# Performance work log

Hardware: AMD Instinct MI355X
Metric: run time of the kernel (lower is better)

## Reference

```python
import jax, jax.numpy as jnp
import numpy as np

EPS = 1e-8  # torch F.cosine_similarity eps


def setup_inputs() -> dict:
    key = jax.random.key(0)
    ks = jax.random.split(key, 12)
    B, S, D, C, V = 2, 1024, 512, 1000, 50000
    sc = lambda fan_in: 1.0 / np.sqrt(fan_in)
    return {
        "spectrum_real": jax.random.normal(ks[0], (B, S, D), jnp.float32),
        "spectrum_imag": jax.random.normal(ks[1], (B, S, D), jnp.float32),
        "concept_spectra_real": jax.random.normal(ks[2], (C, D), jnp.float32),
        "concept_spectra_imag": jax.random.normal(ks[3], (C, D), jnp.float32),
        "W1": jax.random.normal(ks[4], (2 * D, D), jnp.float32) * sc(2 * D),
        "b1": jnp.zeros((D,), jnp.float32),
        "W2": jax.random.normal(ks[5], (D, 512), jnp.float32) * sc(D),
        "b2": jnp.zeros((512,), jnp.float32),
        "W3": jax.random.normal(ks[6], (512, 768), jnp.float32) * sc(512),
        "b3": jnp.zeros((768,), jnp.float32),
        "W4": jax.random.normal(ks[7], (768, V), jnp.float32) * sc(768),
        "b4": jnp.zeros((V,), jnp.float32),
        "top_k": 5,
    }


def reference(spectrum_real, spectrum_imag, concept_spectra_real, concept_spectra_imag,
              W1, b1, W2, b2, W3, b3, W4, b4, top_k):
    # --- find_spectral_matches: batched cosine similarity over magnitudes + top-k ---
    mag = jnp.sqrt(spectrum_real ** 2 + spectrum_imag ** 2)            # [B,S,D]
    cmag = jnp.sqrt(concept_spectra_real ** 2 + concept_spectra_imag ** 2)  # [C,D]
    # cosine sim = (x . y) / (max(||x||, eps) * max(||y||, eps))
    dots = jnp.einsum('bsd,cd->bsc', mag, cmag)                        # [B,S,C]
    xn = jnp.maximum(jnp.linalg.norm(mag, axis=-1), EPS)               # [B,S]
    yn = jnp.maximum(jnp.linalg.norm(cmag, axis=-1), EPS)              # [C]
    sims = dots / (xn[..., None] * yn[None, None, :])                  # [B,S,C]
    top_sims, top_idx = jax.lax.top_k(sims, top_k)                     # [B,S,k]

    # --- decode_spectral_concepts: cat(real, imag) -> MLP -> vocab logits ---
    gelu = lambda x: jax.nn.gelu(x, approximate=False)                 # torch nn.GELU default
    x = jnp.concatenate([spectrum_real, spectrum_imag], axis=-1)       # [B,S,2D]
    h = gelu(x @ W1 + b1)
    h = gelu(h @ W2 + b2)
    h = gelu(h @ W3 + b3)
    logits = h @ W4 + b4                                               # [B,S,V]
    return top_sims, top_idx, logits
```

## Files before the change

### kernel.cpp

```cpp
#include <hip/hip_runtime.h>
#include <hip/hip_bf16.h>
#include <hip/hip_fp8.h>

#define CEPS 1e-8f

typedef __attribute__((ext_vector_type(8))) __bf16 bf16x8;
typedef __attribute__((ext_vector_type(4))) float f32x4;

__device__ __forceinline__ void gload_lds16(const void* g, void* l) {
  __builtin_amdgcn_global_load_lds((const __attribute__((address_space(1))) unsigned int*)g,
                                   (__attribute__((address_space(3))) unsigned int*)l, 16, 0, 0);
}

__device__ __forceinline__ float gelu_f(float v) {
  return 0.5f * v * (1.0f + erff(v * 0.70710678118654752f));
}

__device__ __forceinline__ unsigned char f32_to_e4m3(float v) {
  __hip_fp8_e4m3 t(v);
  return (unsigned char)t.__x;
}


__device__ __forceinline__ void dev_mag(double* red, const float* __restrict__ re,
                                        const float* __restrict__ im, float* __restrict__ mag,
                                        __hip_bfloat16* __restrict__ xcat, float* __restrict__ xn,
                                        int row) {
  const float* r = re + (size_t)row * 512;
  const float* q = im + (size_t)row * 512;
  double ss = 0.0;
  for (int d = threadIdx.x; d < 512; d += 256) {
    float a = r[d], b = q[d];
    float s = __fadd_rn(__fmul_rn(a, a), __fmul_rn(b, b));
    float m = __fsqrt_rn(s);
    mag[(size_t)row * 512 + d] = m;
    xcat[(size_t)row * 1024 + d] = __float2bfloat16(a);
    xcat[(size_t)row * 1024 + 512 + d] = __float2bfloat16(b);
    ss += (double)m * (double)m;
  }
  for (int off = 32; off; off >>= 1) ss += __shfl_xor(ss, off);
  int lane = threadIdx.x & 63, wave = threadIdx.x >> 6;
  if (lane == 0) red[wave] = ss;
  __syncthreads();
  if (threadIdx.x == 0) {
    double tot = red[0] + red[1] + red[2] + red[3];
    float n = (float)sqrt(tot);
    xn[row] = fmaxf(n, CEPS);
  }
}

__device__ __forceinline__ void dev_cmag(double* red, const float* __restrict__ cre,
                                         const float* __restrict__ cim, float* __restrict__ cmagT,
                                         float* __restrict__ yn, int c) {
  const float* r = cre + (size_t)c * 512;
  const float* q = cim + (size_t)c * 512;
  double ss = 0.0;
  for (int d = threadIdx.x; d < 512; d += 256) {
    float a = r[d], b = q[d];
    float s = __fadd_rn(__fmul_rn(a, a), __fmul_rn(b, b));
    float m = __fsqrt_rn(s);
    cmagT[(size_t)d * 1000 + c] = m;
    ss += (double)m * (double)m;
  }
  for (int off = 32; off; off >>= 1) ss += __shfl_xor(ss, off);
  int lane = threadIdx.x & 63, wave = threadIdx.x >> 6;
  if (lane == 0) red[wave] = ss;
  __syncthreads();
  if (threadIdx.x == 0) {
    double tot = red[0] + red[1] + red[2] + red[3];
    float n = (float)sqrt(tot);
    yn[c] = fmaxf(n, CEPS);
  }
}

template <int OUTT>
__device__ __forceinline__ void dev_tr(float (*t32)[65], const float* __restrict__ W,
                                       void* __restrict__ Wt, int K, int N, int bx, int by) {
  int n0 = bx * 64, k0 = by * 64;
  int tid = threadIdx.x;
  {
    int nc = tid & 15, kr4 = tid >> 4;
#pragma unroll
    for (int p = 0; p < 4; ++p) {
      int kr = p * 16 + kr4;
      int n = n0 + nc * 4;
      float4 v = make_float4(0.f, 0.f, 0.f, 0.f);
      if (n < N) v = *(const float4*)(W + (size_t)(k0 + kr) * N + n);
      t32[kr][nc * 4 + 0] = v.x; t32[kr][nc * 4 + 1] = v.y;
      t32[kr][nc * 4 + 2] = v.z; t32[kr][nc * 4 + 3] = v.w;
    }
  }
  __syncthreads();
  {
    int kc = tid & 15, nr4 = tid >> 4;
#pragma unroll
    for (int p = 0; p < 4; ++p) {
      int nr = p * 16 + nr4;
      if (OUTT == 0) {
        ushort4 o;
        __hip_bfloat16 h0 = __float2bfloat16(t32[kc * 4 + 0][nr]);
        __hip_bfloat16 h1 = __float2bfloat16(t32[kc * 4 + 1][nr]);
        __hip_bfloat16 h2 = __float2bfloat16(t32[kc * 4 + 2][nr]);
        __hip_bfloat16 h3 = __float2bfloat16(t32[kc * 4 + 3][nr]);
        o.x = *(unsigned short*)&h0; o.y = *(unsigned short*)&h1;
        o.z = *(unsigned short*)&h2; o.w = *(unsigned short*)&h3;
        *(ushort4*)((unsigned short*)Wt + (size_t)(n0 + nr) * K + k0 + kc * 4) = o;
      } else {
        unsigned int o = (unsigned int)f32_to_e4m3(t32[kc * 4 + 0][nr]) |
                         ((unsigned int)f32_to_e4m3(t32[kc * 4 + 1][nr]) << 8) |
                         ((unsigned int)f32_to_e4m3(t32[kc * 4 + 2][nr]) << 16) |
                         ((unsigned int)f32_to_e4m3(t32[kc * 4 + 3][nr]) << 24);
        *(unsigned int*)((unsigned char*)Wt + (size_t)(n0 + nr) * K + k0 + kc * 4) = o;
      }
    }
  }
}

template <int OUTT>
__device__ __forceinline__ void dev_mlp(short* Al, short* Bl, const __hip_bfloat16* __restrict__ A,
                                        const __hip_bfloat16* __restrict__ Bt, void* __restrict__ C,
                                        int M, int N, int K, int ldc, const float* __restrict__ bias,
                                        int bx, int by) {
  const int tid = threadIdx.x, lane = tid & 63, wave = tid >> 6;
  const int m0 = by * 128, n0 = bx * 128;
  const int wr = wave >> 1, wc = wave & 1;
  f32x4 acc[4][4];
  f32x4 zero4 = {0.f, 0.f, 0.f, 0.f};
#pragma unroll
  for (int i = 0; i < 4; ++i)
#pragma unroll
    for (int j = 0; j < 4; ++j) acc[i][j] = zero4;

  const short* Ag = (const short*)A;
  const short* Bg = (const short*)Bt;
  for (int k0 = 0; k0 < K; k0 += 32) {
#pragma unroll
    for (int s = 0; s < 2; ++s) {
      int seg = wave + s * 4;
      int elem = seg * 512 + lane * 8;
      int row = elem >> 5, kk = elem & 31;
      gload_lds16(Ag + (size_t)(m0 + row) * K + k0 + kk, Al + elem);
      gload_lds16(Bg + (size_t)(n0 + row) * K + k0 + kk, Bl + elem);
    }
    __syncthreads();
    bf16x8 af[4], bfr[4];
    const int fr = lane & 15, fk = (lane >> 4) << 3;
#pragma unroll
    for (int i = 0; i < 4; ++i)
      af[i] = *(const bf16x8*)(Al + (wr * 64 + i * 16 + fr) * 32 + fk);
#pragma unroll
    for (int j = 0; j < 4; ++j)
      bfr[j] = *(const bf16x8*)(Bl + (wc * 64 + j * 16 + fr) * 32 + fk);
#pragma unroll
    for (int i = 0; i < 4; ++i)
#pragma unroll
      for (int j = 0; j < 4; ++j)
        acc[i][j] = __builtin_amdgcn_mfma_f32_16x16x32_bf16(af[i], bfr[j], acc[i][j], 0, 0, 0);
    __syncthreads();
  }
  const int fr = lane & 15, fq = lane >> 4;
#pragma unroll
  for (int j = 0; j < 4; ++j) {
    int col = n0 + wc * 64 + j * 16 + fr;
    if (col >= N) continue;
    float bv = bias[col];
#pragma unroll
    for (int i = 0; i < 4; ++i) {
      int rbase = m0 + wr * 64 + i * 16 + fq * 4;
#pragma unroll
      for (int r = 0; r < 4; ++r) {
        float v = gelu_f(acc[i][j][r] + bv);
        if (OUTT == 0)
          ((__hip_bfloat16*)C)[(size_t)(rbase + r) * ldc + col] = __float2bfloat16(v);
        else
          ((unsigned char*)C)[(size_t)(rbase + r) * ldc + col] = f32_to_e4m3(v);
      }
    }
  }
}

__device__ __forceinline__ void dev_dots(double (*As)[64], double (*Bs)[64],
                                         const float* __restrict__ A, const float* __restrict__ Bm,
                                         float* __restrict__ Cm, int M, int N, int K, int ldc,
                                         const float* __restrict__ xn, const float* __restrict__ yn,
                                         int nb, int mb) {
  const int tid = threadIdx.x;
  const int m0 = mb * 64, n0 = nb * 64;
  const int tx = tid & 15, ty4 = tid >> 4;
  const int ar = tid >> 2, ak = (tid & 3) << 2;
  const int bk = tid >> 4, bn = (tid & 15) << 2;
  double acc[4][4] = {};
  for (int k0 = 0; k0 < K; k0 += 16) {
    float4 a4 = *(const float4*)(A + (size_t)(m0 + ar) * K + k0 + ak);
    As[ak + 0][ar] = (double)a4.x; As[ak + 1][ar] = (double)a4.y;
    As[ak + 2][ar] = (double)a4.z; As[ak + 3][ar] = (double)a4.w;
    float4 b4 = make_float4(0.f, 0.f, 0.f, 0.f);
    if (n0 + bn < N) b4 = *(const float4*)(Bm + (size_t)(k0 + bk) * N + n0 + bn);
    Bs[bk][bn + 0] = (double)b4.x; Bs[bk][bn + 1] = (double)b4.y;
    Bs[bk][bn + 2] = (double)b4.z; Bs[bk][bn + 3] = (double)b4.w;
    __syncthreads();
#pragma unroll
    for (int kk = 0; kk < 16; ++kk) {
      double av[4], bv[4];
#pragma unroll
      for (int i = 0; i < 4; ++i) av[i] = As[kk][ty4 + i * 16];
#pragma unroll
      for (int j = 0; j < 4; ++j) bv[j] = Bs[kk][tx + j * 16];
#pragma unroll
      for (int i = 0; i < 4; ++i)
#pragma unroll
        for (int j = 0; j < 4; ++j)
          acc[i][j] = fma(av[i], bv[j], acc[i][j]);
    }
    __syncthreads();
  }
#pragma unroll
  for (int i = 0; i < 4; ++i) {
    int row = m0 + ty4 + i * 16;
#pragma unroll
    for (int j = 0; j < 4; ++j) {
      int col = n0 + tx + j * 16;
      if (col >= N) continue;
      double d = acc[i][j] / ((double)xn[row] * (double)yn[col]);
      Cm[(size_t)row * ldc + col] = (float)d;
    }
  }
}

__device__ __forceinline__ void dev_gemm(unsigned char (*As)[16384], unsigned char (*Bs)[8192],
                                         const unsigned char* __restrict__ A8,
                                         const unsigned char* __restrict__ B8,
                                         float* __restrict__ C, const float* __restrict__ bias,
                                         int xcd, int j) {
  const int KNT = 12;
  const int Kd = 768, Nd = 50000, ldc = 50000;
  const int tid = threadIdx.x, lane = tid & 63, wave = tid >> 6;
  const int wm = wave >> 1, wn = wave & 1;

  const int mt = j & 7;
  const int ntile = xcd + 8 * (j >> 3);
  const int m0 = mt * 256, n0 = ntile * 128;

  f32x4 acc[8][4];
  f32x4 z4 = {0.f, 0.f, 0.f, 0.f};
#pragma unroll
  for (int q = 0; q < 8; ++q)
#pragma unroll
    for (int p = 0; p < 4; ++p) acc[q][p] = z4;

  auto stageA = [&](int kt, int buf) {
    if (kt >= KNT) return;
    const int k0 = kt * 64;
#pragma unroll
    for (int r = 0; r < 4; ++r) {
      int idx = r * 256 + tid;
      int row = idx >> 2, c = idx & 3;
      int src = ((c * 2) ^ (row & 6)) * 8;
      gload_lds16(A8 + (size_t)(m0 + row) * Kd + k0 + src, &As[buf][row * 64 + c * 16]);
    }
  };
  auto stageB = [&](int kt, int buf) {
    if (kt >= KNT) return;
    const int k0 = kt * 64;
#pragma unroll
    for (int r = 0; r < 2; ++r) {
      int idx = r * 256 + tid;
      int row = idx >> 2, c = idx & 3;
      int src = ((c * 2) ^ (row & 6)) * 8;
      gload_lds16(B8 + (size_t)(n0 + row) * Kd + k0 + src, &Bs[buf][row * 64 + c * 16]);
    }
  };

  stageA(0, 0); stageB(0, 0);
  stageA(1, 1); stageB(1, 1);

  for (int g = 0; g < KNT; ++g) {
    const int buf = g & 1;
    if (g < KNT - 1) asm volatile("s_waitcnt vmcnt(6)" ::: "memory");
    else             asm volatile("s_waitcnt vmcnt(0)" ::: "memory");
    __builtin_amdgcn_sched_barrier(0);
    __builtin_amdgcn_s_barrier();
    __builtin_amdgcn_sched_barrier(0);

    long bfr[4][2];
#pragma unroll
    for (int p = 0; p < 4; ++p) {
      int row = wn * 64 + p * 16 + (lane & 15);
#pragma unroll
      for (int kh = 0; kh < 2; ++kh) {
        int slot = (kh * 4 + (lane >> 4)) ^ (row & 6);
        bfr[p][kh] = *(const long*)(&Bs[buf][row * 64 + slot * 8]);
      }
    }
    __builtin_amdgcn_s_setprio(1);
#pragma unroll
    for (int q = 0; q < 8; ++q) {
      int rowA = wm * 128 + q * 16 + (lane & 15);
      long af[2];
#pragma unroll
      for (int kh = 0; kh < 2; ++kh) {
        int slot = (kh * 4 + (lane >> 4)) ^ (rowA & 6);
        af[kh] = *(const long*)(&As[buf][rowA * 64 + slot * 8]);
      }
#pragma unroll
      for (int kh = 0; kh < 2; ++kh)
#pragma unroll
        for (int p = 0; p < 4; ++p)
          acc[q][p] = __builtin_amdgcn_mfma_f32_16x16x32_fp8_fp8(bfr[p][kh], af[kh], acc[q][p], 0, 0, 0);
    }
    __builtin_amdgcn_s_setprio(0);

    __builtin_amdgcn_sched_barrier(0);
    __builtin_amdgcn_s_barrier();
    __builtin_amdgcn_sched_barrier(0);
    stageA(g + 2, buf);
    stageB(g + 2, buf);
  }

  const int colq = (lane >> 4) * 4;
  float4 bias4[4];
#pragma unroll
  for (int p = 0; p < 4; ++p) {
    int colbase = n0 + wn * 64 + p * 16 + colq;
    bias4[p] = (colbase < Nd) ? *(const float4*)(bias + colbase) : make_float4(0.f, 0.f, 0.f, 0.f);
  }
#pragma unroll
  for (int q = 0; q < 8; ++q) {
    int row = m0 + wm * 128 + q * 16 + (lane & 15);
#pragma unroll
    for (int p = 0; p < 4; ++p) {
      int colbase = n0 + wn * 64 + p * 16 + colq;
      if (colbase < Nd) {
        f32x4 v = acc[q][p];
        float4 o = make_float4(v[0] + bias4[p].x, v[1] + bias4[p].y,
                               v[2] + bias4[p].z, v[3] + bias4[p].w);
        *(float4*)(&C[(size_t)row * ldc + colbase]) = o;
      }
    }
  }
}


__global__ __launch_bounds__(256) void k_pre(const float* W1, __hip_bfloat16* w1t,
                                             const float* W2, __hip_bfloat16* w2t,
                                             const float* W3, __hip_bfloat16* w3t,
                                             const float* cre, const float* cim, float* cmagT, float* yn,
                                             const float* sre, const float* simg, float* mag,
                                             __hip_bfloat16* xcat, float* xn) {
  __shared__ float t32[64][65];
  __shared__ double red[4];
  int bid = blockIdx.x;
  if (bid < 128) {
    dev_tr<0>(t32, W1, (void*)w1t, 1024, 512, bid & 7, bid >> 3);
  } else if (bid < 192) {
    int t = bid - 128;
    dev_tr<0>(t32, W2, (void*)w2t, 512, 512, t & 7, t >> 3);
  } else if (bid < 288) {
    int t = bid - 192;
    dev_tr<0>(t32, W3, (void*)w3t, 512, 768, t % 12, t / 12);
  } else if (bid < 1288) {
    dev_cmag(red, cre, cim, cmagT, yn, bid - 288);
  } else {
    dev_mag(red, sre, simg, mag, xcat, xn, bid - 1288);
  }
}

__global__ __launch_bounds__(256) void k_l1w4(const __hip_bfloat16* xcat, const __hip_bfloat16* w1t,
                                              __hip_bfloat16* h1b, const float* b1,
                                              const float* W4, unsigned char* w4f8) {
  __shared__ short Al[128 * 32];
  __shared__ short Bl[128 * 32];
  __shared__ float t32[64][65];
  int bid = blockIdx.x;
  if (bid < 64) {
    dev_mlp<0>(Al, Bl, xcat, w1t, (void*)h1b, 2048, 512, 1024, 512, b1, bid & 3, bid >> 2);
  } else {
    int t = bid - 64;
    dev_tr<1>(t32, W4, (void*)w4f8, 768, 50000, t % 784, t / 784);
  }
}

template <int OUTT>
__global__ __launch_bounds__(256) void k_mlp(const __hip_bfloat16* A, const __hip_bfloat16* Bt,
                                             void* C, int M, int N, int K, int ldc, const float* bias) {
  __shared__ short Al[128 * 32];
  __shared__ short Bl[128 * 32];
  dev_mlp<OUTT>(Al, Bl, A, Bt, C, M, N, K, ldc, bias, blockIdx.x, blockIdx.y);
}

union KMainSmem {
  struct { unsigned char As[2][16384]; unsigned char Bs[2][8192]; } g;
  struct { double As[16][64]; double Bs[16][64]; } d;
};

__global__ __launch_bounds__(256, 2) void k_main(const unsigned char* __restrict__ A8,
                                                 const unsigned char* __restrict__ B8,
                                                 float* __restrict__ C, const float* __restrict__ bias,
                                                 const float* __restrict__ mag,
                                                 const float* __restrict__ cmagT,
                                                 float* __restrict__ simsb,
                                                 const float* __restrict__ xn,
                                                 const float* __restrict__ yn) {
  __shared__ KMainSmem sm;
  const int bid = blockIdx.x;
  const int g = bid >> 3;
  const bool isDots = ((g % 7) == 3) && (g <= 444);
  if (isDots) {
    int dgi = (g - 3) / 7;
    int id = dgi * 8 + (bid & 7);
    dev_dots(sm.d.As, sm.d.Bs, mag, cmagT, simsb, 2048, 1000, 512, 1000, xn, yn,
             id & 15, id >> 4);
  } else {
    int dots_before = (g < 3) ? 0 : min(64, (g + 4) / 7);
    int jg = g - dots_before;
    dev_gemm(sm.g.As, sm.g.Bs, A8, B8, C, bias, bid & 7, jg);
  }
}

__global__ __launch_bounds__(256) void k_topk(const float* __restrict__ sims,
                                              float* __restrict__ top_sims, float* __restrict__ top_idx) {
  int lane = threadIdx.x & 63, wave = threadIdx.x >> 6;
  int row = blockIdx.x * 4 + wave;
  const float* s = sims + (size_t)row * 1000;
  float v[16];
  int idx[16];
#pragma unroll
  for (int t = 0; t < 16; ++t) {
    int c = lane + t * 64;
    if (c < 1000) { v[t] = s[c]; idx[t] = c; }
    else { v[t] = -1e30f; idx[t] = 1 << 20; }
  }
  for (int j = 0; j < 5; ++j) {
    float bv = -1e30f; int bi = 1 << 20;
#pragma unroll
    for (int t = 0; t < 16; ++t) {
      if (v[t] > bv || (v[t] == bv && idx[t] < bi)) { bv = v[t]; bi = idx[t]; }
    }
    float rv = bv; int ri = bi;
#pragma unroll
    for (int off = 32; off; off >>= 1) {
      float ov = __shfl_xor(rv, off);
      int oi = __shfl_xor(ri, off);
      if (ov > rv || (ov == rv && oi < ri)) { rv = ov; ri = oi; }
    }
    if (lane == 0) {
      top_sims[(size_t)row * 5 + j] = rv;
      top_idx[(size_t)row * 5 + j] = (float)ri;
    }
#pragma unroll
    for (int t = 0; t < 16; ++t)
      if (idx[t] == ri) v[t] = -1e30f;
  }
}

extern "C" void kernel_launch(void* const* d_in, const int* in_sizes, int n_in,
                              void* d_out, int out_size, void* d_ws, size_t ws_size,
                              hipStream_t stream) {
  const float* sre = (const float*)d_in[0];
  const float* simg = (const float*)d_in[1];
  const float* cre = (const float*)d_in[2];
  const float* cim = (const float*)d_in[3];
  const float* W1 = (const float*)d_in[4];
  const float* b1 = (const float*)d_in[5];
  const float* W2 = (const float*)d_in[6];
  const float* b2 = (const float*)d_in[7];
  const float* W3 = (const float*)d_in[8];
  const float* b3 = (const float*)d_in[9];
  const float* W4 = (const float*)d_in[10];
  const float* b4 = (const float*)d_in[11];

  const int M = 2048, D = 512, Cc = 1000, V = 50000, K1 = 1024, H3 = 768;
  const int Npad2 = 392 * 128;

  char* ws = (char*)d_ws;
  size_t off = 0;
  auto alloc = [&](size_t bytes) {
    char* p = ws + off;
    off = (off + bytes + 255) & ~(size_t)255;
    return p;
  };
  __hip_bfloat16* xcatb = (__hip_bfloat16*)alloc((size_t)M * K1 * 2);
  float* mag = (float*)alloc((size_t)M * D * 4);
  float* cmagT = (float*)alloc((size_t)D * Cc * 4);
  float* xn = (float*)alloc((size_t)M * 4);
  float* yn = (float*)alloc((size_t)Cc * 4);
  float* simsb = (float*)alloc((size_t)M * Cc * 4);
  __hip_bfloat16* h1b = (__hip_bfloat16*)alloc((size_t)M * 512 * 2);
  __hip_bfloat16* h2b = (__hip_bfloat16*)alloc((size_t)M * 512 * 2);
  unsigned char* h3f8 = (unsigned char*)alloc((size_t)M * H3);
  __hip_bfloat16* w1t = (__hip_bfloat16*)alloc((size_t)512 * K1 * 2);
  __hip_bfloat16* w2t = (__hip_bfloat16*)alloc((size_t)512 * 512 * 2);
  __hip_bfloat16* w3t = (__hip_bfloat16*)alloc((size_t)H3 * 512 * 2);
  unsigned char* w4f8 = (unsigned char*)alloc((size_t)Npad2 * H3);

  float* top_sims = (float*)d_out;
  float* top_idx = (float*)d_out + (size_t)M * 5;
  float* logits = (float*)d_out + (size_t)M * 5 * 2;

  k_pre<<<dim3(3336), dim3(256), 0, stream>>>(W1, w1t, W2, w2t, W3, w3t,
                                              cre, cim, cmagT, yn, sre, simg, mag, xcatb, xn);
  k_l1w4<<<dim3(64 + 9408), dim3(256), 0, stream>>>(xcatb, w1t, h1b, b1, W4, w4f8);
  k_mlp<0><<<dim3(4, 16), dim3(256), 0, stream>>>(h1b, w2t, (void*)h2b, M, 512, 512, 512, b2);
  k_mlp<1><<<dim3(6, 16), dim3(256), 0, stream>>>(h2b, w3t, (void*)h3f8, M, H3, 512, H3, b3);
  k_main<<<dim3(3648), dim3(256), 0, stream>>>(h3f8, w4f8, logits, b4, mag, cmagT, simsb, xn, yn);
  k_topk<<<dim3(M / 4), dim3(256), 0, stream>>>(simsb, top_sims, top_idx);
}
```

Baseline: 407.2 us.

## Move cosine-dots into L1 kernel and fuse top-k with layer-2 MLP

Moves the fp64 cosine-similarity dot-product blocks out of the big FP8 logits GEMM kernel and into the layer-1/W4-transpose kernel. The top-k selection now runs in the same launch as the layer-2 MLP, which cuts one kernel launch and lets the logits GEMM run without interleaved dots blocks. It also pads the dots LDS tiles to 65 columns to reduce bank conflicts. The cost is that the slow fp64 dots blocks now sit on the path of the earlier small kernels instead of filling gaps in the large GEMM.

```diff
diff --git a/kernel.cpp b/kernel.cpp
--- a/kernel.cpp
+++ b/kernel.cpp
@@ -179,7 +179,7 @@
   }
 }
 
-__device__ __forceinline__ void dev_dots(double (*As)[64], double (*Bs)[64],
+__device__ __forceinline__ void dev_dots(double (*As)[65], double (*Bs)[65],
                                          const float* __restrict__ A, const float* __restrict__ Bm,
                                          float* __restrict__ Cm, int M, int N, int K, int ldc,
                                          const float* __restrict__ xn, const float* __restrict__ yn,
@@ -224,6 +224,43 @@
       double d = acc[i][j] / ((double)xn[row] * (double)yn[col]);
       Cm[(size_t)row * ldc + col] = (float)d;
     }
+  }
+}
+
+__device__ __forceinline__ void dev_topk(const float* __restrict__ sims,
+                                         float* __restrict__ top_sims, float* __restrict__ top_idx,
+                                         int rowblock) {
+  int lane = threadIdx.x & 63, wave = threadIdx.x >> 6;
+  int row = rowblock * 4 + wave;
+  const float* s = sims + (size_t)row * 1000;
+  float v[16];
+  int idx[16];
+#pragma unroll
+  for (int t = 0; t < 16; ++t) {
+    int c = lane + t * 64;
+    if (c < 1000) { v[t] = s[c]; idx[t] = c; }
+    else { v[t] = -1e30f; idx[t] = 1 << 20; }
+  }
+  for (int j = 0; j < 5; ++j) {
+    float bv = -1e30f; int bi = 1 << 20;
+#pragma unroll
+    for (int t = 0; t < 16; ++t) {
+      if (v[t] > bv || (v[t] == bv && idx[t] < bi)) { bv = v[t]; bi = idx[t]; }
+    }
+    float rv = bv; int ri = bi;
+#pragma unroll
+    for (int off = 32; off; off >>= 1) {
+      float ov = __shfl_xor(rv, off);
+      int oi = __shfl_xor(ri, off);
+      if (ov > rv || (ov == rv && oi < ri)) { rv = ov; ri = oi; }
+    }
+    if (lane == 0) {
+      top_sims[(size_t)row * 5 + j] = rv;
+      top_idx[(size_t)row * 5 + j] = (float)ri;
+    }
+#pragma unroll
+    for (int t = 0; t < 16; ++t)
+      if (idx[t] == ri) v[t] = -1e30f;
   }
 }
 
@@ -365,92 +402,56 @@
   }
 }
 
+union L1W4Smem {
+  struct { short Al[128 * 32]; short Bl[128 * 32]; } m;
+  float t32[64][65];
+  struct { double As[16][65]; double Bs[16][65]; } d;
+};
 __global__ __launch_bounds__(256) void k_l1w4(const __hip_bfloat16* xcat, const __hip_bfloat16* w1t,
                                               __hip_bfloat16* h1b, const float* b1,
-                                              const float* W4, unsigned char* w4f8) {
-  __shared__ short Al[128 * 32];
-  __shared__ short Bl[128 * 32];
-  __shared__ float t32[64][65];
+                                              const float* W4, unsigned char* w4f8,
+                                              const float* mag, const float* cmagT, float* simsb,
+                                              const float* xn, const float* yn) {
+  __shared__ L1W4Smem sm;
   int bid = blockIdx.x;
   if (bid < 64) {
-    dev_mlp<0>(Al, Bl, xcat, w1t, (void*)h1b, 2048, 512, 1024, 512, b1, bid & 3, bid >> 2);
-  } else {
-    int t = bid - 64;
-    dev_tr<1>(t32, W4, (void*)w4f8, 768, 50000, t % 784, t / 784);
-  }
-}
-
-template <int OUTT>
-__global__ __launch_bounds__(256) void k_mlp(const __hip_bfloat16* A, const __hip_bfloat16* Bt,
-                                             void* C, int M, int N, int K, int ldc, const float* bias) {
-  __shared__ short Al[128 * 32];
-  __shared__ short Bl[128 * 32];
-  dev_mlp<OUTT>(Al, Bl, A, Bt, C, M, N, K, ldc, bias, blockIdx.x, blockIdx.y);
-}
-
-union KMainSmem {
-  struct { unsigned char As[2][16384]; unsigned char Bs[2][8192]; } g;
-  struct { double As[16][64]; double Bs[16][64]; } d;
-};
-
-__global__ __launch_bounds__(256, 2) void k_main(const unsigned char* __restrict__ A8,
-                                                 const unsigned char* __restrict__ B8,
-                                                 float* __restrict__ C, const float* __restrict__ bias,
-                                                 const float* __restrict__ mag,
-                                                 const float* __restrict__ cmagT,
-                                                 float* __restrict__ simsb,
-                                                 const float* __restrict__ xn,
-                                                 const float* __restrict__ yn) {
-  __shared__ KMainSmem sm;
-  const int bid = blockIdx.x;
-  const int g = bid >> 3;
-  const bool isDots = ((g % 7) == 3) && (g <= 444);
-  if (isDots) {
-    int dgi = (g - 3) / 7;
-    int id = dgi * 8 + (bid & 7);
+    dev_mlp<0>(sm.m.Al, sm.m.Bl, xcat, w1t, (void*)h1b, 2048, 512, 1024, 512, b1, bid & 3, bid >> 2);
+  } else if (bid < 576) {
+    int id = bid - 64;
     dev_dots(sm.d.As, sm.d.Bs, mag, cmagT, simsb, 2048, 1000, 512, 1000, xn, yn,
              id & 15, id >> 4);
   } else {
-    int dots_before = (g < 3) ? 0 : min(64, (g + 4) / 7);
-    int jg = g - dots_before;
-    dev_gemm(sm.g.As, sm.g.Bs, A8, B8, C, bias, bid & 7, jg);
-  }
-}
-
-__global__ __launch_bounds__(256) void k_topk(const float* __restrict__ sims,
-                                              float* __restrict__ top_sims, float* __restrict__ top_idx) {
-  int lane = threadIdx.x & 63, wave = threadIdx.x >> 6;
-  int row = blockIdx.x * 4 + wave;
-  const float* s = sims + (size_t)row * 1000;
-  float v[16];
-  int idx[16];
-#pragma unroll
-  for (int t = 0; t < 16; ++t) {
-    int c = lane + t * 64;
-    if (c < 1000) { v[t] = s[c]; idx[t] = c; }
-    else { v[t] = -1e30f; idx[t] = 1 << 20; }
-  }
-  for (int j = 0; j < 5; ++j) {
-    float bv = -1e30f; int bi = 1 << 20;
-#pragma unroll
-    for (int t = 0; t < 16; ++t) {
-      if (v[t] > bv || (v[t] == bv && idx[t] < bi)) { bv = v[t]; bi = idx[t]; }
-    }
-    float rv = bv; int ri = bi;
-#pragma unroll
-    for (int off = 32; off; off >>= 1) {
-      float ov = __shfl_xor(rv, off);
-      int oi = __shfl_xor(ri, off);
-      if (ov > rv || (ov == rv && oi < ri)) { rv = ov; ri = oi; }
-    }
-    if (lane == 0) {
-      top_sims[(size_t)row * 5 + j] = rv;
-      top_idx[(size_t)row * 5 + j] = (float)ri;
-    }
-#pragma unroll
-    for (int t = 0; t < 16; ++t)
-      if (idx[t] == ri) v[t] = -1e30f;
-  }
+    int t = bid - 576;
+    dev_tr<1>(sm.t32, W4, (void*)w4f8, 768, 50000, t % 784, t / 784);
+  }
+}
+
+__global__ __launch_bounds__(256) void k_l2topk(const __hip_bfloat16* h1b, const __hip_bfloat16* w2t,
+                                                __hip_bfloat16* h2b, const float* b2,
+                                                const float* simsb, float* top_sims, float* top_idx) {
+  __shared__ short Al[128 * 32];
+  __shared__ short Bl[128 * 32];
+  int bid = blockIdx.x;
+  if (bid < 64) {
+    dev_mlp<0>(Al, Bl, h1b, w2t, (void*)h2b, 2048, 512, 512, 512, b2, bid & 3, bid >> 2);
+  } else {
+    dev_topk(simsb, top_sims, top_idx, bid - 64);
+  }
+}
+
+__global__ __launch_bounds__(256) void k_l3(const __hip_bfloat16* h2b, const __hip_bfloat16* w3t,
+                                            unsigned char* h3f8, const float* b3) {
+  __shared__ short Al[128 * 32];
+  __shared__ short Bl[128 * 32];
+  dev_mlp<1>(Al, Bl, h2b, w3t, (void*)h3f8, 2048, 768, 512, 768, b3, blockIdx.x % 6, blockIdx.x / 6);
+}
+
+__global__ __launch_bounds__(256, 2) void k_main(const unsigned char* __restrict__ A8,
+                                                 const unsigned char* __restrict__ B8,
+                                                 float* __restrict__ C, const float* __restrict__ bias) {
+  __shared__ unsigned char As[2][16384];
+  __shared__ unsigned char Bs[2][8192];
+  dev_gemm(As, Bs, A8, B8, C, bias, blockIdx.x & 7, blockIdx.x >> 3);
 }
 
 extern "C" void kernel_launch(void* const* d_in, const int* in_sizes, int n_in,
@@ -499,9 +500,9 @@
 
   k_pre<<<dim3(3336), dim3(256), 0, stream>>>(W1, w1t, W2, w2t, W3, w3t,
                                               cre, cim, cmagT, yn, sre, simg, mag, xcatb, xn);
-  k_l1w4<<<dim3(64 + 9408), dim3(256), 0, stream>>>(xcatb, w1t, h1b, b1, W4, w4f8);
-  k_mlp<0><<<dim3(4, 16), dim3(256), 0, stream>>>(h1b, w2t, (void*)h2b, M, 512, 512, 512, b2);
-  k_mlp<1><<<dim3(6, 16), dim3(256), 0, stream>>>(h2b, w3t, (void*)h3f8, M, H3, 512, H3, b3);
-  k_main<<<dim3(3648), dim3(256), 0, stream>>>(h3f8, w4f8, logits, b4, mag, cmagT, simsb, xn, yn);
-  k_topk<<<dim3(M / 4), dim3(256), 0, stream>>>(simsb, top_sims, top_idx);
-}
+  k_l1w4<<<dim3(64 + 512 + 9408), dim3(256), 0, stream>>>(xcatb, w1t, h1b, b1, W4, w4f8,
+                                                          mag, cmagT, simsb, xn, yn);
+  k_l2topk<<<dim3(64 + 512), dim3(256), 0, stream>>>(h1b, w2t, h2b, b2, simsb, top_sims, top_idx);
+  k_l3<<<dim3(96), dim3(256), 0, stream>>>(h2b, w3t, h3f8, b3);
+  k_main<<<dim3(3136), dim3(256), 0, stream>>>(h3f8, w4f8, logits, b4);
+}
```

Result: faster. 390.2 us (-4.2%).
